# Performance work log

Measured on AMD Instinct MI355X. Metric: run time of the kernel, lower is better.

## Reference

```python
import jax, jax.numpy as jnp
import numpy as np

N, D, H = 4096, 512, 8
HD = D // H
KEEP_RATIO = 0.5
EPS = 1e-6

def setup_inputs() -> dict:
    key = jax.random.key(0)
    ks = jax.random.split(key, 10)
    s = 1.0 / np.sqrt(D)
    return {
        'stock_feats': jax.random.normal(ks[0], (N, D), jnp.float32),
        'z_primary': jax.random.normal(ks[1], (1, D), jnp.float32),
        'z_secondary': jax.random.normal(ks[2], (1, D), jnp.float32),
        'Wq': jax.random.normal(ks[3], (D, D), jnp.float32) * s,
        'Wk': jax.random.normal(ks[4], (D, D), jnp.float32) * s,
        'Wv': jax.random.normal(ks[5], (D, D), jnp.float32) * s,
        'Wg': jax.random.normal(ks[6], (D, 2 * D), jnp.float32) * s,
        'bg': jnp.zeros((D,), jnp.float32),
        'Wag': jax.random.normal(ks[7], (D, 2 * D), jnp.float32) * s,
        'bag': jnp.zeros((D,), jnp.float32),
        'norm_w': jnp.ones((D,), jnp.float32),
        'Wo': jax.random.normal(ks[8], (D, D), jnp.float32) * s,
        'bo': jnp.zeros((D,), jnp.float32),
    }

def reference(stock_feats, z_primary, z_secondary, Wq, Wk, Wv, Wg, bg, Wag, bag, norm_w, Wo, bo):
    scale = 1.0 / np.sqrt(HD)
    nodes = jnp.concatenate([z_primary, z_secondary, stock_feats], axis=0)  # [N+2, D]
    # regime-gated queries
    z_concat = jnp.concatenate([z_primary, z_secondary], axis=-1)  # [1, 2D]
    regime_mod = jax.nn.sigmoid(z_concat @ Wg.T + bg)              # [1, D]
    q = ((stock_feats @ Wq.T) * regime_mod).reshape(N, H, HD)
    k = (nodes @ Wk.T).reshape(N + 2, H, HD)
    v = (nodes @ Wv.T).reshape(N + 2, H, HD)
    scores = jnp.einsum('nhd,mhd->nhm', q, k) * scale              # [N, H, N+2]
    raw_scores = scores.mean(axis=1)                               # [N, N+2]
    # top-k mask over stock (non-anchor) columns
    anchor_scores = scores[..., :2]
    stock_scores = scores[..., 2:]                                 # [N, H, N]
    k_keep = max(5, int(N * KEEP_RATIO))
    topk_val = jax.lax.top_k(stock_scores, k_keep)[0]
    threshold = topk_val[..., -1:]
    stock_scores = jnp.where(stock_scores >= threshold, stock_scores, -1e9)
    scores_m = jnp.concatenate([anchor_scores, stock_scores], axis=-1)
    attn = jax.nn.softmax(scores_m, axis=-1)                       # [N, H, N+2]
    out = jnp.einsum('nhm,mhd->nhd', attn, v).reshape(N, D)
    out = out @ Wo.T + bo
    # alpha guard: gated residual + RMSNorm
    gate = jax.nn.sigmoid(jnp.concatenate([stock_feats, out], axis=-1) @ Wag.T + bag)
    gr = stock_feats + gate * out
    rms = jax.lax.rsqrt(jnp.mean(gr * gr, axis=-1, keepdims=True) + EPS)
    final_out = gr * rms * norm_w
    return (final_out, raw_scores, gate.mean(), attn.mean(axis=1))
```

## Files before the change

### kernel.cpp

```cpp
#include <hip/hip_runtime.h>
#include <hip/hip_fp16.h>
#include <math.h>

#define NS 4096
#define DIM 512
#define NH 8
#define HD 64
#define M2 4098
#define MPAD 4224
#define KKEEP 2048u

#define OUT_F 0
#define OUT_R 2097152
#define OUT_G 18882560
#define OUT_A 18882561

typedef __attribute__((ext_vector_type(8))) short bf16x8;
typedef __attribute__((ext_vector_type(4))) float f32x4;

__device__ __forceinline__ float sigmoidf_(float x) { return 1.0f / (1.0f + __expf(-x)); }

__device__ __forceinline__ unsigned short btrunc(float f) {
  unsigned u = __float_as_uint(f);
  u = u + 0x7FFFu + ((u >> 16) & 1u);
  return (unsigned short)(u >> 16);
}
__device__ __forceinline__ float bton(unsigned short h) {
  return __uint_as_float(((unsigned)h) << 16);
}

__device__ __forceinline__ void scan_pick(unsigned c0, unsigned c1, unsigned c2, unsigned c3,
                                          unsigned k_rem, int lane,
                                          unsigned& bsel_out, unsigned& nxt_out) {
  unsigned run = c0 + c1 + c2 + c3;
  #pragma unroll
  for (int off = 1; off < 64; off <<= 1) {
    unsigned o_ = __shfl_down(run, off, 64);
    if (lane + off < 64) run += o_;
  }
  unsigned s0 = run, s1 = run - c0, s2 = s1 - c1, s3 = s2 - c2, s4 = s3 - c3;
  int which = -1;
  if      (s0 >= k_rem && s1 < k_rem) which = 0;
  else if (s1 >= k_rem && s2 < k_rem) which = 1;
  else if (s2 >= k_rem && s3 < k_rem) which = 2;
  else if (s3 >= k_rem && s4 < k_rem) which = 3;
  unsigned long long bal = __ballot(which >= 0);
  int src = (int)__ffsll(bal) - 1;
  unsigned nxtv = (which == 0) ? s1 : (which == 1) ? s2 : (which == 2) ? s3 : s4;
  unsigned bsel = (unsigned)(4 * lane + (which < 0 ? 0 : which));
  bsel_out = (unsigned)__shfl((int)bsel, src, 64);
  nxt_out  = (unsigned)__shfl((int)nxtv, src, 64);
}

__global__ __launch_bounds__(256) void regime_kernel(
    const float* __restrict__ zp, const float* __restrict__ zs,
    const float* __restrict__ Wg, const float* __restrict__ bg,
    float* __restrict__ regime) {
  __shared__ float zc[1024];
  int t = threadIdx.x;
  for (int i = t; i < 512; i += 256) { zc[i] = zp[i]; zc[512 + i] = zs[i]; }
  __syncthreads();
  for (int j = t; j < 512; j += 256) {
    const float4* w = (const float4*)(Wg + (size_t)j * 1024);
    float acc = 0.f;
    #pragma unroll 8
    for (int i = 0; i < 256; i++) {
      float4 wv = w[i];
      acc += wv.x * zc[4*i] + wv.y * zc[4*i+1] + wv.z * zc[4*i+2] + wv.w * zc[4*i+3];
    }
    regime[j] = sigmoidf_(acc + bg[j]);
  }
}

__global__ __launch_bounds__(256) void conv_bf(
    const float* __restrict__ src, unsigned short* __restrict__ dst, int n4) {
  int i4 = blockIdx.x * 256 + threadIdx.x;
  if (i4 >= n4) return;
  float4 v = *(const float4*)(src + (size_t)i4 * 4);
  ushort4 o; o.x = btrunc(v.x); o.y = btrunc(v.y); o.z = btrunc(v.z); o.w = btrunc(v.w);
  *(ushort4*)(dst + (size_t)i4 * 4) = o;
}

__global__ __launch_bounds__(256) void build_nodes_bf(
    const float* __restrict__ zp, const float* __restrict__ zs,
    const float* __restrict__ sf, unsigned short* __restrict__ nb) {
  int i4 = blockIdx.x * 256 + threadIdx.x;
  if (i4 >= (M2 * DIM) / 4) return;
  int idx = i4 * 4;
  int m = idx >> 9, c = idx & 511;
  const float* src = (m == 0) ? (zp + c) : (m == 1) ? (zs + c)
                               : (sf + (size_t)(m - 2) * 512 + c);
  float4 v = *(const float4*)src;
  ushort4 o; o.x = btrunc(v.x); o.y = btrunc(v.y); o.z = btrunc(v.z); o.w = btrunc(v.w);
  *(ushort4*)(nb + idx) = o;
}

#define LSTR 40
__global__ __launch_bounds__(256) void gemm_bf16(
    const unsigned short* __restrict__ A, const unsigned short* __restrict__ B,
    const float* __restrict__ bias, const float* __restrict__ cscale,
    float* __restrict__ Cf, unsigned short* __restrict__ Cb,
    int M, int N, int K, int lda, int ldb, int ldc, float scale, int mode,
    size_t sA, size_t sB, size_t sC) {
  __shared__ unsigned short As[128 * LSTR];
  __shared__ unsigned short Bs[128 * LSTR];
  const int z = blockIdx.z;
  A += (size_t)z * sA;
  B += (size_t)z * sB;
  if (Cf) Cf += (size_t)z * sC;
  if (Cb) Cb += (size_t)z * sC;
  const int t = threadIdx.x;
  const int w = t >> 6, lane = t & 63;
  const int wr = w >> 1, wc = w & 1;
  const int lr = lane & 15, lg = lane >> 4;
  const int bm = blockIdx.y * 128, bn = blockIdx.x * 128;
  f32x4 acc[4][4] = {};
  for (int k0 = 0; k0 < K; k0 += 32) {
    #pragma unroll
    for (int i = 0; i < 2; i++) {
      int q = t + i * 256;
      int row = q >> 2;
      int ko = (q & 3) * 8;
      bf16x8 av = {};
      int gr = bm + row;
      if (gr < M) av = *(const bf16x8*)(A + (size_t)gr * lda + k0 + ko);
      *(bf16x8*)(As + row * LSTR + ko) = av;
      bf16x8 bv = {};
      int gbr = bn + row;
      if (gbr < N) bv = *(const bf16x8*)(B + (size_t)gbr * ldb + k0 + ko);
      *(bf16x8*)(Bs + row * LSTR + ko) = bv;
    }
    __syncthreads();
    {
      bf16x8 af[4], bfr[4];
      #pragma unroll
      for (int i = 0; i < 4; i++)
        af[i] = *(const bf16x8*)(As + (64 * wr + 16 * i + lr) * LSTR + lg * 8);
      #pragma unroll
      for (int j = 0; j < 4; j++)
        bfr[j] = *(const bf16x8*)(Bs + (64 * wc + 16 * j + lr) * LSTR + lg * 8);
      #pragma unroll
      for (int i = 0; i < 4; i++)
        #pragma unroll
        for (int j = 0; j < 4; j++)
          acc[i][j] = __builtin_amdgcn_mfma_f32_16x16x32_bf16(af[i], bfr[j], acc[i][j], 0, 0, 0);
    }
    __syncthreads();
  }
  #pragma unroll
  for (int i = 0; i < 4; i++) {
    #pragma unroll
    for (int j = 0; j < 4; j++) {
      #pragma unroll
      for (int q = 0; q < 4; q++) {
        int row = bm + 64 * wr + 16 * i + lg * 4 + q;
        int col = bn + 64 * wc + 16 * j + lr;
        if (row < M && col < N) {
          float v = acc[i][j][q] * scale;
          if (bias)   v += bias[col];
          if (cscale) v *= cscale[col];
          if (mode == 0)      Cf[(size_t)row * ldc + col] = v;
          else if (mode == 1) Cb[(size_t)row * ldc + col] = btrunc(v);
          else                Cb[(size_t)col * ldc + row] = btrunc(v);
        }
      }
    }
  }
}

__global__ __launch_bounds__(256) void select_softmax(unsigned short* __restrict__ S) {
  __shared__ unsigned short keys[4][MPAD];
  __shared__ unsigned hist[4][256];
  const int w = threadIdx.x >> 6, lane = threadIdx.x & 63;
  const size_t row = (size_t)blockIdx.x * 4 + w;
  unsigned short* kr = keys[w];
  unsigned* hw = hist[w];
  unsigned short* g = S + row * MPAD;
  unsigned a0k = 0, a1k = 0;

  #pragma unroll
  for (int c = 0; c < 9; ++c) {
    if (c < 8 || lane < 16) {
      uint4 v = *(const uint4*)(g + c * 512 + lane * 8);
      unsigned* pv = (unsigned*)&v;
      int mb = c * 512 + lane * 8;
      #pragma unroll
      for (int p2 = 0; p2 < 4; ++p2) {
        unsigned pk = pv[p2], outw = 0;
        #pragma unroll
        for (int e = 0; e < 2; ++e) {
          int m = mb + 2 * p2 + e;
          unsigned u = (e == 0) ? (pk & 0xFFFFu) : (pk >> 16);
          unsigned key = u ^ ((u & 0x8000u) ? 0xFFFFu : 0x8000u);
          if (m < 2) { if (m == 0) a0k = key; else a1k = key; key = 0u; }
          else if (m >= M2) key = 0u;
          outw |= key << (16 * e);
        }
        *(unsigned*)(kr + mb + 2 * p2) = outw;
      }
    }
  }

  hw[lane] = 0u; hw[lane + 64] = 0u; hw[lane + 128] = 0u; hw[lane + 192] = 0u;
  unsigned maxkey = (lane == 0) ? ((a0k > a1k) ? a0k : a1k) : 0u;
  #pragma unroll
  for (int c = 0; c < 9; ++c) {
    if (c < 8 || lane < 16) {
      uint4 v = *(const uint4*)(kr + c * 512 + lane * 8);
      const unsigned* pv = (const unsigned*)&v;
      #pragma unroll
      for (int p2 = 0; p2 < 4; ++p2) {
        unsigned lo = pv[p2] & 0xFFFFu, hi = pv[p2] >> 16;
        atomicAdd(&hw[lo >> 8], 1u);
        atomicAdd(&hw[hi >> 8], 1u);
        if (lo > maxkey) maxkey = lo;
        if (hi > maxkey) maxkey = hi;
      }
    }
  }
  #pragma unroll
  for (int off = 32; off > 0; off >>= 1) {
    unsigned o_ = (unsigned)__shfl_xor((int)maxkey, off, 64);
    if (o_ > maxkey) maxkey = o_;
  }
  float lmax = bton((unsigned short)(maxkey ^ ((maxkey & 0x8000u) ? 0x8000u : 0xFFFFu)));

  unsigned tb, k_rem = KKEEP;
  {
    unsigned c0 = hw[4*lane], c1 = hw[4*lane+1], c2 = hw[4*lane+2], c3 = hw[4*lane+3];
    unsigned nxtv;
    scan_pick(c0, c1, c2, c3, k_rem, lane, tb, nxtv);
    k_rem -= nxtv;
  }

  hw[lane] = 0u; hw[lane + 64] = 0u; hw[lane + 128] = 0u; hw[lane + 192] = 0u;
  #pragma unroll
  for (int c = 0; c < 9; ++c) {
    if (c < 8 || lane < 16) {
      uint4 v = *(const uint4*)(kr + c * 512 + lane * 8);
      const unsigned* pv = (const unsigned*)&v;
      #pragma unroll
      for (int p2 = 0; p2 < 4; ++p2) {
        unsigned lo = pv[p2] & 0xFFFFu, hi = pv[p2] >> 16;
        if ((lo >> 8) == tb) atomicAdd(&hw[lo & 255u], 1u);
        if ((hi >> 8) == tb) atomicAdd(&hw[hi & 255u], 1u);
      }
    }
  }
  unsigned thrkey;
  {
    unsigned c0 = hw[4*lane], c1 = hw[4*lane+1], c2 = hw[4*lane+2], c3 = hw[4*lane+3];
    unsigned bsel, nxtv;
    scan_pick(c0, c1, c2, c3, k_rem, lane, bsel, nxtv);
    thrkey = (tb << 8) | bsel;
  }

  float lsum = 0.f;
  #pragma unroll
  for (int c = 0; c < 9; ++c) {
    if (c < 8 || lane < 16) {
      uint4 v = *(const uint4*)(kr + c * 512 + lane * 8);
      unsigned* pv = (unsigned*)&v;
      #pragma unroll
      for (int p2 = 0; p2 < 4; ++p2) {
        unsigned pk = pv[p2], outw = 0;
        bool anc = (c == 0 && lane == 0 && p2 == 0);
        if (anc) pk = a0k | (a1k << 16);
        #pragma unroll
        for (int e = 0; e < 2; ++e) {
          unsigned key = (e == 0) ? (pk & 0xFFFFu) : (pk >> 16);
          bool kept = anc || (key >= thrkey);
          unsigned short us = (unsigned short)(key ^ ((key & 0x8000u) ? 0x8000u : 0xFFFFu));
          float ev = kept ? __expf(bton(us) - lmax) : 0.f;
          unsigned short eb = btrunc(ev);
          lsum += bton(eb);
          outw |= ((unsigned)eb) << (16 * e);
        }
        pv[p2] = outw;
      }
      *(uint4*)(kr + c * 512 + lane * 8) = v;
    }
  }
  #pragma unroll
  for (int off = 32; off > 0; off >>= 1) lsum += __shfl_xor(lsum, off, 64);
  float invZ = 1.0f / lsum;

  #pragma unroll
  for (int c = 0; c < 9; ++c) {
    if (c < 8 || lane < 16) {
      uint4 v = *(const uint4*)(kr + c * 512 + lane * 8);
      unsigned* pv = (unsigned*)&v;
      #pragma unroll
      for (int p2 = 0; p2 < 4; ++p2) {
        unsigned pk = pv[p2];
        float pf0 = bton((unsigned short)(pk & 0xFFFFu)) * invZ;
        float pf1 = bton((unsigned short)(pk >> 16)) * invZ;
        pv[p2] = (unsigned)btrunc(pf0) | (((unsigned)btrunc(pf1)) << 16);
      }
      *(uint4*)(g + c * 512 + lane * 8) = v;
    }
  }
}

__global__ __launch_bounds__(256) void am_reduce(
    const unsigned short* __restrict__ P, float* __restrict__ outA) {
  int tid = blockIdx.x * 256 + threadIdx.x;
  int n = tid / 513, cm = tid % 513;
  int bm = cm * 8;
  float s[8] = {};
  #pragma unroll
  for (int h = 0; h < 8; ++h) {
    uint4 v = *(const uint4*)(P + ((size_t)h * 4096 + n) * MPAD + bm);
    const unsigned* pv = (const unsigned*)&v;
    #pragma unroll
    for (int p2 = 0; p2 < 4; ++p2) {
      s[2*p2]   += bton((unsigned short)(pv[p2] & 0xFFFFu));
      s[2*p2+1] += bton((unsigned short)(pv[p2] >> 16));
    }
  }
  float* dst = outA + (size_t)n * M2 + bm;
  #pragma unroll
  for (int k = 0; k < 8; ++k)
    if (bm + k < M2) dst[k] = s[k] * 0.125f;
}

#define SROWB 8464
#define QOFF  (16 * SROWB)
#define HOFF  (QOFF + 16 * 72 * 2)
#define AOFF  (HOFF + 16 * 256 * 4)
#define SMEMSZ (AOFF + 64)

__global__ __launch_bounds__(1024) void fused_attn(
    const unsigned short* __restrict__ Qbf, const unsigned short* __restrict__ Kbf,
    const unsigned short* __restrict__ Vt, unsigned short* __restrict__ aobf,
    float* __restrict__ attn_mean_out) {
  extern __shared__ char dsm[];
  unsigned short* qt = (unsigned short*)(dsm + QOFF);
  unsigned* hist = (unsigned*)(dsm + HOFF);
  unsigned short* anchk = (unsigned short*)(dsm + AOFF);
  const int n0 = blockIdx.x * 16;
  const int t = threadIdx.x;
  const int w = t >> 6, lane = t & 63;
  const int lr = lane & 15, lg = lane >> 4;
  unsigned* hw = hist + w * 256;
  const int r = w;
  const unsigned swz = (unsigned)((r & 7) << 4);

  for (int h = 0; h < NH; ++h) {
    qt[(t >> 6) * 72 + (t & 63)] = Qbf[(size_t)(n0 + (t >> 6)) * DIM + h * HD + (t & 63)];
    __syncthreads();
    {
      bf16x8 a0 = *(const bf16x8*)(qt + lr * 72 + lg * 8);
      bf16x8 a1 = *(const bf16x8*)(qt + lr * 72 + 32 + lg * 8);
      #pragma unroll
      for (int f = 0; f < 17; ++f) {
        if (f < 16 || w < 8) {
          int m0 = (w + 16 * f) * 16;
          const unsigned short* kp = Kbf + (size_t)(m0 + lr) * DIM + h * HD + lg * 8;
          bf16x8 b0 = *(const bf16x8*)(kp);
          bf16x8 b1 = *(const bf16x8*)(kp + 32);
          f32x4 c = {0.f, 0.f, 0.f, 0.f};
          c = __builtin_amdgcn_mfma_f32_16x16x32_bf16(a0, b0, c, 0, 0, 0);
          c = __builtin_amdgcn_mfma_f32_16x16x32_bf16(a1, b1, c, 0, 0, 0);
          int m = m0 + lr;
          #pragma unroll
          for (int q = 0; q < 4; ++q) {
            int rr = lg * 4 + q;
            unsigned short us = btrunc(c[q] * 0.125f);
            unsigned key = (unsigned)us ^ ((us & 0x8000u) ? 0xFFFFu : 0x8000u);
            unsigned short stor = (m >= M2 || m < 2) ? (unsigned short)0 : (unsigned short)key;
            *(unsigned short*)(dsm + rr * SROWB + ((2 * m) ^ ((rr & 7) << 4))) = stor;
            if (m < 2) anchk[rr * 2 + m] = (unsigned short)key;
          }
        }
      }
    }
    __syncthreads();

    float invZ;
    {
      unsigned maxkey = 0;
      hw[lane] = 0u; hw[lane + 64] = 0u; hw[lane + 128] = 0u; hw[lane + 192] = 0u;
      #pragma unroll
      for (int c = 0; c < 9; ++c) {
        if (c < 8 || lane < 16) {
          uint4 pk4 = *(const uint4*)(dsm + r * SROWB + (((unsigned)(c * 1024 + lane * 16)) ^ swz));
          const unsigned* pw = (const unsigned*)&pk4;
          #pragma unroll
          for (int p2 = 0; p2 < 4; ++p2) {
            unsigned pk = pw[p2];
            unsigned lo = pk & 0xFFFFu, hi = pk >> 16;
            atomicAdd(&hw[lo >> 8], 1u);
            atomicAdd(&hw[hi >> 8], 1u);
            if (lo > maxkey) maxkey = lo;
            if (hi > maxkey) maxkey = hi;
          }
        }
      }
      #pragma unroll
      for (int off = 32; off > 0; off >>= 1) {
        unsigned o_ = (unsigned)__shfl_xor((int)maxkey, off, 64);
        if (o_ > maxkey) maxkey = o_;
      }
      {
        unsigned a0 = anchk[2 * r], a1 = anchk[2 * r + 1];
        if (a0 > maxkey) maxkey = a0;
        if (a1 > maxkey) maxkey = a1;
      }
      float lmax = bton((unsigned short)(maxkey ^ ((maxkey & 0x8000u) ? 0x8000u : 0xFFFFu)));

      unsigned tb, k_rem = KKEEP;
      {
        unsigned c0 = hw[4*lane], c1 = hw[4*lane+1], c2 = hw[4*lane+2], c3 = hw[4*lane+3];
        unsigned nxtv;
        scan_pick(c0, c1, c2, c3, k_rem, lane, tb, nxtv);
        k_rem -= nxtv;
      }
      hw[lane] = 0u; hw[lane + 64] = 0u; hw[lane + 128] = 0u; hw[lane + 192] = 0u;
      #pragma unroll
      for (int c = 0; c < 9; ++c) {
        if (c < 8 || lane < 16) {
          uint4 pk4 = *(const uint4*)(dsm + r * SROWB + (((unsigned)(c * 1024 + lane * 16)) ^ swz));
          const unsigned* pw = (const unsigned*)&pk4;
          #pragma unroll
          for (int p2 = 0; p2 < 4; ++p2) {
            unsigned pk = pw[p2];
            unsigned lo = pk & 0xFFFFu, hi = pk >> 16;
            if ((lo >> 8) == tb) atomicAdd(&hw[lo & 255u], 1u);
            if ((hi >> 8) == tb) atomicAdd(&hw[hi & 255u], 1u);
          }
        }
      }
      unsigned thrkey;
      {
        unsigned c0 = hw[4*lane], c1 = hw[4*lane+1], c2 = hw[4*lane+2], c3 = hw[4*lane+3];
        unsigned bsel, nxtv;
        scan_pick(c0, c1, c2, c3, k_rem, lane, bsel, nxtv);
        thrkey = (tb << 8) | bsel;
      }

      float lsum = 0.f;
      #pragma unroll
      for (int c = 0; c < 9; ++c) {
        if (c < 8 || lane < 16) {
          char* ap = dsm + r * SROWB + (((unsigned)(c * 1024 + lane * 16)) ^ swz);
          uint4 pk4 = *(const uint4*)ap;
          unsigned* pw = (unsigned*)&pk4;
          #pragma unroll
          for (int p2 = 0; p2 < 4; ++p2) {
            unsigned pk = pw[p2];
            bool anc = (c == 0 && lane == 0 && p2 == 0);
            if (anc) pk = (unsigned)anchk[2 * r] | ((unsigned)anchk[2 * r + 1] << 16);
            unsigned outw = 0;
            #pragma unroll
            for (int e = 0; e < 2; ++e) {
              unsigned key = (e == 0) ? (pk & 0xFFFFu) : (pk >> 16);
              bool kept = anc || (key >= thrkey);
              unsigned short us = (unsigned short)(key ^ ((key & 0x8000u) ? 0x8000u : 0xFFFFu));
              float evf = kept ? __expf(bton(us) - lmax) : 0.f;
              unsigned short eb = btrunc(evf);
              lsum += bton(eb);
              outw |= ((unsigned)eb) << (16 * e);
            }
            pw[p2] = outw;
          }
          *(uint4*)ap = pk4;
        }
      }
      #pragma unroll
      for (int off = 32; off > 0; off >>= 1) lsum += __shfl_xor(lsum, off, 64);
      invZ = 1.0f / lsum;
      for (int c = 0; c < 9; ++c) {
        if (c < 8 || lane < 16) {
          const char* ap = dsm + r * SROWB + (((unsigned)(c * 1024 + lane * 16)) ^ swz);
          uint4 e4 = *(const uint4*)ap;
          const unsigned* pw = (const unsigned*)&e4;
          int bm = c * 512 + lane * 8;
          float* base = attn_mean_out + (size_t)(n0 + r) * M2 + bm;
          #pragma unroll
          for (int p2 = 0; p2 < 4; ++p2) {
            float v0 = bton((unsigned short)(pw[p2] & 0xFFFFu)) * invZ * 0.125f;
            float v1 = bton((unsigned short)(pw[p2] >> 16)) * invZ * 0.125f;
            int m = bm + 2 * p2;
            if (m < M2)     { if (h == 0) base[2*p2] = v0;   else base[2*p2] += v0; }
            if (m + 1 < M2) { if (h == 0) base[2*p2+1] = v1; else base[2*p2+1] += v1; }
          }
        }
      }
    }
    __syncthreads();

    {
      f32x4 o0 = {0.f,0.f,0.f,0.f}, o1 = o0, o2 = o0, o3 = o0;
      const unsigned short* Vb = Vt + (size_t)(h * HD) * MPAD;
      #pragma unroll
      for (int ks = 0; ks < 9; ++ks) {
        if (ks < 8 || w < 4) {
          int kk = (w + 16 * ks) * 32 + lg * 8;
          bf16x8 a = *(const bf16x8*)(dsm + lr * SROWB + ((2 * kk) ^ ((lr & 7) << 4)));
          {
            bf16x8 b0 = *(const bf16x8*)(Vb + (size_t)(lr) * MPAD + kk);
            bf16x8 b1 = *(const bf16x8*)(Vb + (size_t)(16 + lr) * MPAD + kk);
            o0 = __builtin_amdgcn_mfma_f32_16x16x32_bf16(a, b0, o0, 0, 0, 0);
            o1 = __builtin_amdgcn_mfma_f32_16x16x32_bf16(a, b1, o1, 0, 0, 0);
          }
          {
            bf16x8 b2 = *(const bf16x8*)(Vb + (size_t)(32 + lr) * MPAD + kk);
            bf16x8 b3 = *(const bf16x8*)(Vb + (size_t)(48 + lr) * MPAD + kk);
            o2 = __builtin_amdgcn_mfma_f32_16x16x32_bf16(a, b2, o2, 0, 0, 0);
            o3 = __builtin_amdgcn_mfma_f32_16x16x32_bf16(a, b3, o3, 0, 0, 0);
          }
        }
      }
      __syncthreads();
      float* part = (float*)dsm;
      #pragma unroll
      for (int q = 0; q < 4; q++) {
        int row = lg * 4 + q;
        part[w * 1024 + row * 64 +      lr] = o0[q];
        part[w * 1024 + row * 64 + 16 + lr] = o1[q];
        part[w * 1024 + row * 64 + 32 + lr] = o2[q];
        part[w * 1024 + row * 64 + 48 + lr] = o3[q];
      }
      __syncthreads();
      {
        float s = 0.f;
        #pragma unroll
        for (int ww = 0; ww < 16; ++ww) s += part[ww * 1024 + t];
        aobf[(size_t)(n0 + (t >> 6)) * DIM + h * HD + (t & 63)] = btrunc(s * invZ);
      }
    }
  }
}

__global__ __launch_bounds__(256) void cat_bf(
    const unsigned short* __restrict__ sfbf, const float* __restrict__ pj,
    unsigned short* __restrict__ cat) {
  int i4 = blockIdx.x * 256 + threadIdx.x;
  if (i4 >= (4096 * 1024) / 4) return;
  int idx = i4 * 4;
  int n = idx >> 10, c = idx & 1023;
  if (c < 512) {
    *(ushort4*)(cat + idx) = *(const ushort4*)(sfbf + (size_t)n * 512 + c);
  } else {
    float4 v = *(const float4*)(pj + (size_t)n * 512 + (c - 512));
    ushort4 o; o.x = btrunc(v.x); o.y = btrunc(v.y); o.z = btrunc(v.z); o.w = btrunc(v.w);
    *(ushort4*)(cat + idx) = o;
  }
}

__global__ __launch_bounds__(256) void final_kernel(
    const float* __restrict__ sf, const float* __restrict__ pj,
    const float* __restrict__ gl, const float* __restrict__ norm_w,
    float* __restrict__ outf, float* __restrict__ gpart) {
  int n = blockIdx.x, t = threadIdx.x;
  __shared__ float red[256];
  size_t base = (size_t)n * 512;
  float g0 = sigmoidf_(gl[base + t]);
  float g1 = sigmoidf_(gl[base + 256 + t]);
  float x0 = sf[base + t], x1 = sf[base + 256 + t];
  float p0 = pj[base + t], p1 = pj[base + 256 + t];
  float gr0 = x0 + g0 * p0, gr1 = x1 + g1 * p1;

  red[t] = g0 + g1;
  __syncthreads();
  for (int off = 128; off > 0; off >>= 1) {
    if (t < off) red[t] += red[t + off];
    __syncthreads();
  }
  if (t == 0) gpart[n] = red[0];
  __syncthreads();

  red[t] = gr0 * gr0 + gr1 * gr1;
  __syncthreads();
  for (int off = 128; off > 0; off >>= 1) {
    if (t < off) red[t] += red[t + off];
    __syncthreads();
  }
  float rms = rsqrtf(red[0] * (1.0f / 512.0f) + 1e-6f);
  outf[base + t] = gr0 * rms * norm_w[t];
  outf[base + 256 + t] = gr1 * rms * norm_w[256 + t];
}

__global__ __launch_bounds__(256) void gate_reduce(
    const float* __restrict__ gpart, float* __restrict__ out_scalar) {
  __shared__ float red[256];
  int t = threadIdx.x;
  float s = 0.f;
  for (int i = t; i < 4096; i += 256) s += gpart[i];
  red[t] = s;
  __syncthreads();
  for (int off = 128; off > 0; off >>= 1) {
    if (t < off) red[t] += red[t + off];
    __syncthreads();
  }
  if (t == 0) out_scalar[0] = red[0] * (1.0f / (4096.0f * 512.0f));
}

extern "C" void kernel_launch(void* const* d_in, const int* in_sizes, int n_in,
                              void* d_out, int out_size, void* d_ws, size_t ws_size,
                              hipStream_t stream) {
  const float* sf  = (const float*)d_in[0];
  const float* zp  = (const float*)d_in[1];
  const float* zs  = (const float*)d_in[2];
  const float* Wq  = (const float*)d_in[3];
  const float* Wk  = (const float*)d_in[4];
  const float* Wv  = (const float*)d_in[5];
  const float* Wg  = (const float*)d_in[6];
  const float* bg  = (const float*)d_in[7];
  const float* Wag = (const float*)d_in[8];
  const float* bag = (const float*)d_in[9];
  const float* nw  = (const float*)d_in[10];
  const float* Wo  = (const float*)d_in[11];
  const float* bo  = (const float*)d_in[12];

  float* out  = (float*)d_out;
  float* outF = out + OUT_F;
  float* outR = out + OUT_R;
  float* outG = out + OUT_G;
  float* outA = out + OUT_A;

  char* W = (char*)d_ws;
  float*          regime  = (float*)(W + 0);
  float*          gpart   = (float*)(W + 2048);
  unsigned short* sfbf    = (unsigned short*)(W + 18432);
  unsigned short* nodesbf = (unsigned short*)(W + 4212736);
  unsigned short* Qbf     = (unsigned short*)(W + 8409088);
  unsigned short* Kbf     = (unsigned short*)(W + 12603392);
  unsigned short* Vt      = (unsigned short*)(W + 16928768);
  unsigned short* aobf    = (unsigned short*)(W + 21254144);
  unsigned short* catbf   = (unsigned short*)(W + 25448448);
  unsigned short* Wqbf    = (unsigned short*)(W + 33837056);
  unsigned short* Wkbf    = (unsigned short*)(W + 34361344);
  unsigned short* Wvbf    = (unsigned short*)(W + 34885632);
  unsigned short* Wobf    = (unsigned short*)(W + 35409920);
  unsigned short* Wagbf   = (unsigned short*)(W + 35934208);
  float*          pj      = (float*)(W + 36982784);
  float*          gl      = (float*)(W + 4212736);
  unsigned short* Splane  = (unsigned short*)(W + 45371392);
  const size_t need_s = 45371392ull + (size_t)8 * 4096 * MPAD * 2;
  const int use_s = (ws_size >= need_s) ? 1 : 0;

  hipFuncSetAttribute((const void*)fused_attn,
                      hipFuncAttributeMaxDynamicSharedMemorySize, SMEMSZ);

  regime_kernel<<<1, 256, 0, stream>>>(zp, zs, Wg, bg, regime);
  conv_bf<<<2048, 256, 0, stream>>>(sf, sfbf, 524288);
  build_nodes_bf<<<2049, 256, 0, stream>>>(zp, zs, sf, nodesbf);
  conv_bf<<<256, 256, 0, stream>>>(Wq, Wqbf, 65536);
  conv_bf<<<256, 256, 0, stream>>>(Wk, Wkbf, 65536);
  conv_bf<<<256, 256, 0, stream>>>(Wv, Wvbf, 65536);
  conv_bf<<<256, 256, 0, stream>>>(Wo, Wobf, 65536);
  conv_bf<<<512, 256, 0, stream>>>(Wag, Wagbf, 131072);
  hipMemsetAsync(Kbf, 0, 4325376, stream);
  hipMemsetAsync(Vt, 0, 4325376, stream);

  gemm_bf16<<<dim3(4, 32, 1), 256, 0, stream>>>(sfbf, Wqbf, nullptr, regime, nullptr, Qbf,
                                                4096, 512, 512, 512, 512, 512, 1.0f, 1, 0, 0, 0);
  gemm_bf16<<<dim3(4, 33, 1), 256, 0, stream>>>(nodesbf, Wkbf, nullptr, nullptr, nullptr, Kbf,
                                                M2, 512, 512, 512, 512, 512, 1.0f, 1, 0, 0, 0);
  gemm_bf16<<<dim3(4, 33, 1), 256, 0, stream>>>(nodesbf, Wvbf, nullptr, nullptr, nullptr, Vt,
                                                M2, 512, 512, 512, 512, MPAD, 1.0f, 2, 0, 0, 0);

  gemm_bf16<<<dim3(33, 32, 1), 256, 0, stream>>>(Qbf, Kbf, nullptr, nullptr, outR, nullptr,
                                                 4096, M2, 512, 512, 512, M2, 0.015625f, 0, 0, 0, 0);

  if (use_s) {
    gemm_bf16<<<dim3(33, 32, 8), 256, 0, stream>>>(Qbf, Kbf, nullptr, nullptr, nullptr, Splane,
                                                   4096, M2, 64, 512, 512, MPAD, 0.125f, 1,
                                                   64, 64, (size_t)4096 * MPAD);
    select_softmax<<<8192, 256, 0, stream>>>(Splane);
    gemm_bf16<<<dim3(1, 32, 8), 256, 0, stream>>>(Splane, Vt, nullptr, nullptr, nullptr, aobf,
                                                  4096, 64, MPAD, MPAD, MPAD, 512, 1.0f, 1,
                                                  (size_t)4096 * MPAD, (size_t)64 * MPAD, 64);
    am_reduce<<<8208, 256, 0, stream>>>(Splane, outA);
  } else {
    fused_attn<<<256, 1024, SMEMSZ, stream>>>(Qbf, Kbf, Vt, aobf, outA);
  }

  gemm_bf16<<<dim3(4, 32, 1), 256, 0, stream>>>(aobf, Wobf, bo, nullptr, pj, nullptr,
                                                4096, 512, 512, 512, 512, 512, 1.0f, 0, 0, 0, 0);
  cat_bf<<<4096, 256, 0, stream>>>(sfbf, pj, catbf);
  gemm_bf16<<<dim3(4, 32, 1), 256, 0, stream>>>(catbf, Wagbf, bag, nullptr, gl, nullptr,
                                                4096, 512, 1024, 1024, 1024, 512, 1.0f, 0, 0, 0, 0);
  final_kernel<<<4096, 256, 0, stream>>>(sf, pj, gl, nw, outF, gpart);
  gate_reduce<<<1, 256, 0, stream>>>(gpart, outG);
}
```

Baseline: 911.7 us.

## Defer softmax normalization to consumers and fuse histogram into key pass

The select_softmax kernel no longer runs a final pass that multiplies every probability by 1/Z. It writes the unnormalized exponentials straight to global memory and stores 1/Z per row in a new buffer, Zg. The P·V GEMM applies that value as a row scale in its epilogue, and am_reduce multiplies by it while accumulating. The first histogram and max pass is also merged into the key-building loop, removing one more LDS sweep per row. The risk is small numeric drift, since values are rounded to bf16 before normalization, and the workspace threshold now also covers the Zg buffer.

```diff
diff --git a/kernel.cpp b/kernel.cpp
--- a/kernel.cpp
+++ b/kernel.cpp
@@ -99,9 +99,10 @@
 __global__ __launch_bounds__(256) void gemm_bf16(
     const unsigned short* __restrict__ A, const unsigned short* __restrict__ B,
     const float* __restrict__ bias, const float* __restrict__ cscale,
+    const float* __restrict__ rscale,
     float* __restrict__ Cf, unsigned short* __restrict__ Cb,
     int M, int N, int K, int lda, int ldb, int ldc, float scale, int mode,
-    size_t sA, size_t sB, size_t sC) {
+    size_t sA, size_t sB, size_t sC, size_t sR) {
   __shared__ unsigned short As[128 * LSTR];
   __shared__ unsigned short Bs[128 * LSTR];
   const int z = blockIdx.z;
@@ -109,6 +110,7 @@
   B += (size_t)z * sB;
   if (Cf) Cf += (size_t)z * sC;
   if (Cb) Cb += (size_t)z * sC;
+  if (rscale) rscale += (size_t)z * sR;
   const int t = threadIdx.x;
   const int w = t >> 6, lane = t & 63;
   const int wr = w >> 1, wc = w & 1;
@@ -159,6 +161,7 @@
           float v = acc[i][j][q] * scale;
           if (bias)   v += bias[col];
           if (cscale) v *= cscale[col];
+          if (rscale) v *= rscale[row];
           if (mode == 0)      Cf[(size_t)row * ldc + col] = v;
           else if (mode == 1) Cb[(size_t)row * ldc + col] = btrunc(v);
           else                Cb[(size_t)col * ldc + row] = btrunc(v);
@@ -168,7 +171,8 @@
   }
 }
 
-__global__ __launch_bounds__(256) void select_softmax(unsigned short* __restrict__ S) {
+__global__ __launch_bounds__(256) void select_softmax(
+    unsigned short* __restrict__ S, float* __restrict__ Zg) {
   __shared__ unsigned short keys[4][MPAD];
   __shared__ unsigned hist[4][256];
   const int w = threadIdx.x >> 6, lane = threadIdx.x & 63;
@@ -178,6 +182,8 @@
   unsigned short* g = S + row * MPAD;
   unsigned a0k = 0, a1k = 0;
 
+  hw[lane] = 0u; hw[lane + 64] = 0u; hw[lane + 128] = 0u; hw[lane + 192] = 0u;
+  unsigned maxkey = 0;
   #pragma unroll
   for (int c = 0; c < 9; ++c) {
     if (c < 8 || lane < 16) {
@@ -195,29 +201,15 @@
           if (m < 2) { if (m == 0) a0k = key; else a1k = key; key = 0u; }
           else if (m >= M2) key = 0u;
           outw |= key << (16 * e);
+          atomicAdd(&hw[key >> 8], 1u);
+          if (key > maxkey) maxkey = key;
         }
         *(unsigned*)(kr + mb + 2 * p2) = outw;
       }
     }
   }
-
-  hw[lane] = 0u; hw[lane + 64] = 0u; hw[lane + 128] = 0u; hw[lane + 192] = 0u;
-  unsigned maxkey = (lane == 0) ? ((a0k > a1k) ? a0k : a1k) : 0u;
-  #pragma unroll
-  for (int c = 0; c < 9; ++c) {
-    if (c < 8 || lane < 16) {
-      uint4 v = *(const uint4*)(kr + c * 512 + lane * 8);
-      const unsigned* pv = (const unsigned*)&v;
-      #pragma unroll
-      for (int p2 = 0; p2 < 4; ++p2) {
-        unsigned lo = pv[p2] & 0xFFFFu, hi = pv[p2] >> 16;
-        atomicAdd(&hw[lo >> 8], 1u);
-        atomicAdd(&hw[hi >> 8], 1u);
-        if (lo > maxkey) maxkey = lo;
-        if (hi > maxkey) maxkey = hi;
-      }
-    }
-  }
+  if (a0k > maxkey) maxkey = a0k;
+  if (a1k > maxkey) maxkey = a1k;
   #pragma unroll
   for (int off = 32; off > 0; off >>= 1) {
     unsigned o_ = (unsigned)__shfl_xor((int)maxkey, off, 64);
@@ -278,44 +270,30 @@
         }
         pv[p2] = outw;
       }
-      *(uint4*)(kr + c * 512 + lane * 8) = v;
+      *(uint4*)(g + c * 512 + lane * 8) = v;
     }
   }
   #pragma unroll
   for (int off = 32; off > 0; off >>= 1) lsum += __shfl_xor(lsum, off, 64);
-  float invZ = 1.0f / lsum;
-
-  #pragma unroll
-  for (int c = 0; c < 9; ++c) {
-    if (c < 8 || lane < 16) {
-      uint4 v = *(const uint4*)(kr + c * 512 + lane * 8);
-      unsigned* pv = (unsigned*)&v;
-      #pragma unroll
-      for (int p2 = 0; p2 < 4; ++p2) {
-        unsigned pk = pv[p2];
-        float pf0 = bton((unsigned short)(pk & 0xFFFFu)) * invZ;
-        float pf1 = bton((unsigned short)(pk >> 16)) * invZ;
-        pv[p2] = (unsigned)btrunc(pf0) | (((unsigned)btrunc(pf1)) << 16);
-      }
-      *(uint4*)(g + c * 512 + lane * 8) = v;
-    }
-  }
+  if (lane == 0) Zg[row] = 1.0f / lsum;
 }
 
 __global__ __launch_bounds__(256) void am_reduce(
-    const unsigned short* __restrict__ P, float* __restrict__ outA) {
+    const unsigned short* __restrict__ P, const float* __restrict__ Zg,
+    float* __restrict__ outA) {
   int tid = blockIdx.x * 256 + threadIdx.x;
   int n = tid / 513, cm = tid % 513;
   int bm = cm * 8;
   float s[8] = {};
   #pragma unroll
   for (int h = 0; h < 8; ++h) {
+    float zi = Zg[h * 4096 + n];
     uint4 v = *(const uint4*)(P + ((size_t)h * 4096 + n) * MPAD + bm);
     const unsigned* pv = (const unsigned*)&v;
     #pragma unroll
     for (int p2 = 0; p2 < 4; ++p2) {
-      s[2*p2]   += bton((unsigned short)(pv[p2] & 0xFFFFu));
-      s[2*p2+1] += bton((unsigned short)(pv[p2] >> 16));
+      s[2*p2]   += bton((unsigned short)(pv[p2] & 0xFFFFu)) * zi;
+      s[2*p2+1] += bton((unsigned short)(pv[p2] >> 16)) * zi;
     }
   }
   float* dst = outA + (size_t)n * M2 + bm;
@@ -638,7 +616,8 @@
   float*          pj      = (float*)(W + 36982784);
   float*          gl      = (float*)(W + 4212736);
   unsigned short* Splane  = (unsigned short*)(W + 45371392);
-  const size_t need_s = 45371392ull + (size_t)8 * 4096 * MPAD * 2;
+  float*          Zg      = (float*)(W + 322195456);
+  const size_t need_s = 322195456ull + 131072ull;
   const int use_s = (ws_size >= need_s) ? 1 : 0;
 
   hipFuncSetAttribute((const void*)fused_attn,
@@ -655,34 +634,34 @@
   hipMemsetAsync(Kbf, 0, 4325376, stream);
   hipMemsetAsync(Vt, 0, 4325376, stream);
 
-  gemm_bf16<<<dim3(4, 32, 1), 256, 0, stream>>>(sfbf, Wqbf, nullptr, regime, nullptr, Qbf,
-                                                4096, 512, 512, 512, 512, 512, 1.0f, 1, 0, 0, 0);
-  gemm_bf16<<<dim3(4, 33, 1), 256, 0, stream>>>(nodesbf, Wkbf, nullptr, nullptr, nullptr, Kbf,
-                                                M2, 512, 512, 512, 512, 512, 1.0f, 1, 0, 0, 0);
-  gemm_bf16<<<dim3(4, 33, 1), 256, 0, stream>>>(nodesbf, Wvbf, nullptr, nullptr, nullptr, Vt,
-                                                M2, 512, 512, 512, 512, MPAD, 1.0f, 2, 0, 0, 0);
-
-  gemm_bf16<<<dim3(33, 32, 1), 256, 0, stream>>>(Qbf, Kbf, nullptr, nullptr, outR, nullptr,
-                                                 4096, M2, 512, 512, 512, M2, 0.015625f, 0, 0, 0, 0);
+  gemm_bf16<<<dim3(4, 32, 1), 256, 0, stream>>>(sfbf, Wqbf, nullptr, regime, nullptr, nullptr, Qbf,
+                                                4096, 512, 512, 512, 512, 512, 1.0f, 1, 0, 0, 0, 0);
+  gemm_bf16<<<dim3(4, 33, 1), 256, 0, stream>>>(nodesbf, Wkbf, nullptr, nullptr, nullptr, nullptr, Kbf,
+                                                M2, 512, 512, 512, 512, 512, 1.0f, 1, 0, 0, 0, 0);
+  gemm_bf16<<<dim3(4, 33, 1), 256, 0, stream>>>(nodesbf, Wvbf, nullptr, nullptr, nullptr, nullptr, Vt,
+                                                M2, 512, 512, 512, 512, MPAD, 1.0f, 2, 0, 0, 0, 0);
+
+  gemm_bf16<<<dim3(33, 32, 1), 256, 0, stream>>>(Qbf, Kbf, nullptr, nullptr, nullptr, outR, nullptr,
+                                                 4096, M2, 512, 512, 512, M2, 0.015625f, 0, 0, 0, 0, 0);
 
   if (use_s) {
-    gemm_bf16<<<dim3(33, 32, 8), 256, 0, stream>>>(Qbf, Kbf, nullptr, nullptr, nullptr, Splane,
+    gemm_bf16<<<dim3(33, 32, 8), 256, 0, stream>>>(Qbf, Kbf, nullptr, nullptr, nullptr, nullptr, Splane,
                                                    4096, M2, 64, 512, 512, MPAD, 0.125f, 1,
-                                                   64, 64, (size_t)4096 * MPAD);
-    select_softmax<<<8192, 256, 0, stream>>>(Splane);
-    gemm_bf16<<<dim3(1, 32, 8), 256, 0, stream>>>(Splane, Vt, nullptr, nullptr, nullptr, aobf,
+                                                   64, 64, (size_t)4096 * MPAD, 0);
+    select_softmax<<<8192, 256, 0, stream>>>(Splane, Zg);
+    gemm_bf16<<<dim3(1, 32, 8), 256, 0, stream>>>(Splane, Vt, nullptr, nullptr, Zg, nullptr, aobf,
                                                   4096, 64, MPAD, MPAD, MPAD, 512, 1.0f, 1,
-                                                  (size_t)4096 * MPAD, (size_t)64 * MPAD, 64);
-    am_reduce<<<8208, 256, 0, stream>>>(Splane, outA);
+                                                  (size_t)4096 * MPAD, (size_t)64 * MPAD, 64, 4096);
+    am_reduce<<<8208, 256, 0, stream>>>(Splane, Zg, outA);
   } else {
     fused_attn<<<256, 1024, SMEMSZ, stream>>>(Qbf, Kbf, Vt, aobf, outA);
   }
 
-  gemm_bf16<<<dim3(4, 32, 1), 256, 0, stream>>>(aobf, Wobf, bo, nullptr, pj, nullptr,
-                                                4096, 512, 512, 512, 512, 512, 1.0f, 0, 0, 0, 0);
+  gemm_bf16<<<dim3(4, 32, 1), 256, 0, stream>>>(aobf, Wobf, bo, nullptr, nullptr, pj, nullptr,
+                                                4096, 512, 512, 512, 512, 512, 1.0f, 0, 0, 0, 0, 0);
   cat_bf<<<4096, 256, 0, stream>>>(sfbf, pj, catbf);
-  gemm_bf16<<<dim3(4, 32, 1), 256, 0, stream>>>(catbf, Wagbf, bag, nullptr, gl, nullptr,
-                                                4096, 512, 1024, 1024, 1024, 512, 1.0f, 0, 0, 0, 0);
+  gemm_bf16<<<dim3(4, 32, 1), 256, 0, stream>>>(catbf, Wagbf, bag, nullptr, nullptr, gl, nullptr,
+                                                4096, 512, 1024, 1024, 1024, 512, 1.0f, 0, 0, 0, 0, 0);
   final_kernel<<<4096, 256, 0, stream>>>(sf, pj, gl, nw, outF, gpart);
   gate_reduce<<<1, 256, 0, stream>>>(gpart, outG);
 }
```

Measured after the change: 922.0 us. No clear change (+1.1%).
